# Optimization experiments

Measured on AMD Instinct MI355X. Metric: run time of the kernel, lower is better.

The kernel has to match this reference:

```python
import jax, jax.numpy as jnp
import numpy as np

NEG = -100.0
# Transition index layout from DecoderPHMM cat order
M2M, M2I, M2D, I2M, I2I, D2M, D2D = 0, 1, 2, 3, 4, 5, 6
LOG_QUARTER = float(np.log(0.25))


def _d_chain(fM, a):
    """Delete-state recurrence along motif axis k for one sequence column.
    fD[0] = NEG; fD[k] = logaddexp(a[k-1,M2D] + fM[k-1], a[k-1,D2D] + fD[k-1]).
    fM: (B, K+1), a: (B, K+1, 7) -> (B, K+1)."""
    B, Kp1 = fM.shape
    K = Kp1 - 1

    def step(fD_prev, inp):
        am2d, ad2d, fMk = inp  # each (B,)
        fD = jnp.logaddexp(am2d + fMk, ad2d + fD_prev)
        return fD, fD

    init = jnp.full((B,), NEG, dtype=fM.dtype)
    inputs = (a[:, :K, M2D].T, a[:, :K, D2D].T, fM[:, :K].T)  # (K, B) each
    _, fDs = jax.lax.scan(step, init, inputs)
    return jnp.concatenate([init[:, None], fDs.T], axis=1)  # (B, K+1)


def _profile_hmm_loss(transition_probs, emission_probs, batch_input):
    """Profile-HMM forward algorithm in log space, vectorized over batch.
    transition_probs: (B, K+1, 7) log; emission_probs: (B, K, 4) log;
    batch_input: (B, L) int tokens in [0,4). Returns (B,) NLL."""
    a = transition_probs
    e_m = emission_probs
    B, Kp1, _ = a.shape
    K = Kp1 - 1
    b_idx = jnp.arange(B)
    k_idx = jnp.arange(K)

    # Column l = 0: f[M,0,0] = 0, rest -100; I stays -100; D chain over k.
    fM0 = jnp.full((B, Kp1), NEG, dtype=a.dtype).at[:, 0].set(0.0)
    fI0 = jnp.full((B, Kp1), NEG, dtype=a.dtype)
    fD0 = _d_chain(fM0, a)

    def col_step(carry, sym):
        fM, fI, fD = carry  # each (B, K+1), previous column l-1
        # emission e_m[b, k, sym[b]] -> (B, K)
        em = e_m[b_idx[:, None], k_idx[None, :], sym[:, None]]
        prev = jnp.stack([a[:, :K, M2M] + fM[:, :K],
                          a[:, :K, I2M] + fI[:, :K],
                          a[:, :K, D2M] + fD[:, :K]], axis=0)  # (3, B, K)
        fM_new = jnp.concatenate(
            [jnp.full((B, 1), NEG, dtype=a.dtype),
             em + jax.scipy.special.logsumexp(prev, axis=0)], axis=1)
        fI_new = LOG_QUARTER + jnp.logaddexp(a[:, :, M2I] + fM,
                                             a[:, :, I2I] + fI)
        fD_new = _d_chain(fM_new, a)  # uses current-column M values
        return (fM_new, fI_new, fD_new), None

    (fM, fI, fD), _ = jax.lax.scan(col_step, (fM0, fI0, fD0), batch_input.T)

    final = jnp.stack([fM[:, K] + a[:, K, M2M],
                       fI[:, K] + a[:, K, I2M],
                       fD[:, K] + a[:, K, D2M]], axis=0)  # (3, B)
    return -jax.scipy.special.logsumexp(final, axis=0)


def _kld_loss(mus, logvars):
    return -0.5 * jnp.sum(1.0 + logvars - mus ** 2 - jnp.exp(logvars), axis=1)


def setup_inputs() -> dict:
    key = jax.random.key(0)
    k1, k2, k3, k4, k5 = jax.random.split(key, 5)
    B, L, K, E = 512, 256, 128, 16
    batch_input = jax.random.randint(k1, (B, L), 0, 4)
    transition_probs = jax.random.normal(k2, (B, K + 1, 7), dtype=jnp.float32)
    emission_probs = jax.random.normal(k3, (B, K, 4), dtype=jnp.float32)
    mus = jax.random.normal(k4, (B, E), dtype=jnp.float32)
    logvars = jax.random.normal(k5, (B, E), dtype=jnp.float32)
    return {"batch_input": batch_input, "transition_probs": transition_probs,
            "emission_probs": emission_probs, "mus": mus, "logvars": logvars}


def reference(batch_input, transition_probs, emission_probs, mus, logvars):
    beta = 1.0
    recon = _profile_hmm_loss(transition_probs, emission_probs, batch_input).mean()
    kld = _kld_loss(mus, logvars).mean()
    return recon + beta * kld
```

## Files before the change

kernel.cpp:

```cpp
#include <hip/hip_runtime.h>


constexpr float LOG2E = 1.4426950408889634f;
constexpr float LN2   = 0.6931471805599453f;

__device__ __forceinline__ float exp2_hw(float x){ return __builtin_amdgcn_exp2f(x); }
__device__ __forceinline__ float log2_hw(float x){ return __builtin_amdgcn_logf(x); }
__device__ __forceinline__ float ldx(float x,int e){ return __builtin_amdgcn_ldexpf(x,e); }
__device__ __forceinline__ int   fxe(float x){ return __builtin_amdgcn_frexp_expf(x); }
__device__ __forceinline__ int   dppi(int o,int s){ return __builtin_amdgcn_update_dpp(o,s,0x138,0xF,0xF,false); }
__device__ __forceinline__ float dppf(float o,float s){ return __int_as_float(dppi(__float_as_int(o),__float_as_int(s))); }

#define STEP(FRESH, ISS1, MASKED, SM1) do {                                    \
                    \
    const float qmM = dppf(0.0f, emM);              \
    const float qmI = dppf(0.0f, emI);                                         \
    const float qmD = dppf(0.0f, emD);                                         \
    const float qeM = dppf(0.0f, cMy);              \
    const float qeI = dppf(0.0f, cIy);                                         \
    const float qeD = dppf(0.0f, cDy);                                         \
    const int   qE  = dppi(E, E);          \
    const int qsym  = dppi((FRESH), symq);                                     \
                \
    const float v   = (ISS1) ? q1g : gg * u;                    \
    const float nI1 = fmaf(tmi1, cMx, tii1 * cIx);                             \
    const float nI2 = fmaf(tmi2, cMy, tii2 * cIy);                             \
    const float sq  = ldx(1.0f, qE - E);                                       \
    const float sp  = ldx(1.0f, pE - E);                                       \
    const float tPI = ldx(u, EI0 - E);               \
    const float tmI = ldx(v, EI0 - E);                                         \
                  \
    const float mM  = qmM * sq;                          \
    const float mD  = qmD * sq;                                                \
    const float eM_ = qeM * sq;                                                \
    const float eD_ = qeD * sq;                                                \
    const float PM  = pM * sp;             \
    const float PD  = pD * sp;                                                 \
    const float mI  = lane0 ? tmI : qmI * sq;                                  \
    const float PI  = lane0 ? tPI : pI * sp;                                   \
                                               \
    const bool ba = (qsym & 1) != 0, bb = (qsym & 2) != 0;                     \
    const bool bc = (qsym & 4) != 0, bd = (qsym & 8) != 0;                     \
    const float e1c = bb ? (ba ? el1.w : el1.z) : (ba ? el1.y : el1.x);        \
    const float e2c = bb ? (ba ? el2.w : el2.z) : (ba ? el2.y : el2.x);        \
    const float e1d = bd ? (bc ? el1.w : el1.z) : (bc ? el1.y : el1.x);        \
    const float e2d = bd ? (bc ? el2.w : el2.z) : (bc ? el2.y : el2.x);        \
                                                          \
    const float nM1 = e1c * fmaf(tdm0, PD,  fmaf(tim0, PI,  tmm0 * PM));       \
    const float nM2 = e2c * fmaf(tdm1, cDx, fmaf(tim1, cIx, tmm1 * cMx));      \
    const float nD1 = fmaf(tmd0, mM, tdd0 * mD);                               \
    const float nD2 = fmaf(tmd1, nM1, tdd1 * nD1);                             \
                                                        \
    const float nM1b = e1d * fmaf(tdm0, mD,  fmaf(tim0, mI,  tmm0 * mM));      \
    const float nI1b = fmaf(tmi1, nM1, tii1 * nI1);                            \
    const float nI2b = fmaf(tmi2, nM2, tii2 * nI2);                            \
    const float nD1b = fmaf(tmd0, eM_, tdd0 * eD_);                            \
    const float nM2b = e2d * fmaf(tdm1, nD1, fmaf(tim1, nI1, tmm1 * nM1));     \
    const float nD2b = fmaf(tmd1, nM1b, tdd1 * nD1b);                          \
                                                         \
    emM = nM2; emI = nI2; emD = nD2;               \
    if (MASKED) {                                                              \
        const bool act = ((unsigned)((SM1) - i)) < 128u;                       \
        cMx = act ? nM1b : cMx;  cMy = act ? nM2b : cMy;                       \
        cIx = act ? nI1b : cIx;  cIy = act ? nI2b : cIy;                       \
        cDx = act ? nD1b : cDx;  cDy = act ? nD2b : cDy;                       \
    } else {                                                                   \
        cMx = nM1b; cMy = nM2b; cIx = nI1b; cIy = nI2b; cDx = nD1b; cDy = nD2b;\
    }                                                                          \
    pM = qeM; pI = qeI; pD = qeD; pE = qE;                                     \
    symq = qsym;                                                               \
    u = gg * v;                                                   \
} while (0)

#define RESCALE do {                                                           \
    const float anc = fmaxf(fmaxf(fmaxf(cMx, cMy), fmaxf(cIx, cIy)),           \
                            fmaxf(cDx, cDy));                                  \
    const int e = fxe(anc);                                                    \
    E += e;                                                                    \
    const float sE = ldx(1.0f, -e);                                            \
    cMx *= sE; cMy *= sE; cIx *= sE; cIy *= sE; cDx *= sE; cDy *= sE;          \
    emM *= sE; emI *= sE; emD *= sE;                                           \
    const int eI = fxe(u); EI0 += eI; u = ldx(u, -eI);                         \
} while (0)

__global__ __launch_bounds__(64, 1) void phmm_fwd(const int* __restrict__ tokens,
                                                  const float* __restrict__ trans,
                                                  const float* __restrict__ emis,
                                                  float* __restrict__ nll_out)
{
    const int b = blockIdx.x;
    const int i = threadIdx.x;
    const bool lane0 = (i == 0);

    const float* ab = trans + (size_t)b * 903;
    const int r0 = (2*i)*7, r1 = (2*i+1)*7, r2 = (2*i+2)*7;

    const float tmm0 = exp2_hw(ab[r0+0]*LOG2E);
    const float tim0 = exp2_hw(ab[r0+3]*LOG2E);
    const float tdm0 = exp2_hw(ab[r0+5]*LOG2E);
    const float tmd0 = exp2_hw(ab[r0+2]*LOG2E);
    const float tdd0 = exp2_hw(ab[r0+6]*LOG2E);
    const float tmm1 = exp2_hw(ab[r1+0]*LOG2E);
    const float tim1 = exp2_hw(ab[r1+3]*LOG2E);
    const float tdm1 = exp2_hw(ab[r1+5]*LOG2E);
    const float tmd1 = exp2_hw(ab[r1+2]*LOG2E);
    const float tdd1 = exp2_hw(ab[r1+6]*LOG2E);
    const float tmi1 = 0.25f*exp2_hw(ab[r1+1]*LOG2E);
    const float tii1 = 0.25f*exp2_hw(ab[r1+4]*LOG2E);
    const float tmi2 = 0.25f*exp2_hw(ab[r2+1]*LOG2E);
    const float tii2 = 0.25f*exp2_hw(ab[r2+4]*LOG2E);
    const float q1g  = 0.25f*exp2_hw(ab[1]*LOG2E);
    const float gg   = 0.25f*exp2_hw(ab[4]*LOG2E);
    const float tKmm = exp2_hw(ab[128*7+0]*LOG2E);
    const float tKim = exp2_hw(ab[128*7+3]*LOG2E);
    const float tKdm = exp2_hw(ab[128*7+5]*LOG2E);

    const float4* eb = (const float4*)(emis + (size_t)b*512);
    float4 el1 = eb[2*i], el2 = eb[2*i+1];
    el1.x=exp2_hw(el1.x*LOG2E); el1.y=exp2_hw(el1.y*LOG2E);
    el1.z=exp2_hw(el1.z*LOG2E); el1.w=exp2_hw(el1.w*LOG2E);
    el2.x=exp2_hw(el2.x*LOG2E); el2.y=exp2_hw(el2.y*LOG2E);
    el2.z=exp2_hw(el2.z*LOG2E); el2.w=exp2_hw(el2.w*LOG2E);

    const int4 ts = ((const int4*)(tokens + (size_t)b*256))[i];

    const float ldd0 = ab[r0+6]*LOG2E;
    const float ldd1 = ab[r1+6]*LOG2E;
    const float lmd0b = ab[2]*LOG2E;
    float incl = (lane0 ? 0.0f : ldd0) + ldd1;
    #pragma unroll
    for (int d = 1; d < 64; d <<= 1) {
        float t = __shfl_up(incl, d);
        if (i >= d) incl += t;
    }
    float exPre = __shfl_up(incl, 1);
    if (lane0) exPre = 0.0f;
    const float g1 = lmd0b + exPre + (lane0 ? 0.0f : ldd0);
    const float g2 = g1 + ldd1;

    int E = (int)floorf(fmaxf(g1, g2));
    float cMx = 0.0f, cMy = 0.0f, cIx = 0.0f, cIy = 0.0f;
    float cDx = exp2_hw(g1 - (float)E), cDy = exp2_hw(g2 - (float)E);
    float emM = 0.0f, emI = 0.0f, emD = 0.0f;
    float pM = lane0 ? 1.0f : 0.0f;
    float pI = 0.0f, pD = 0.0f; int pE = 0;
    float u = 0.0f; int EI0 = 0;
    int symq = 0;

    #pragma unroll 1
    for (int g = 0; g < 16; ++g) {
        const int a0 = __builtin_amdgcn_readlane(ts.x, 2*g);
        const int a1 = __builtin_amdgcn_readlane(ts.y, 2*g);
        const int a2 = __builtin_amdgcn_readlane(ts.z, 2*g);
        const int a3 = __builtin_amdgcn_readlane(ts.w, 2*g);
        const int b0 = __builtin_amdgcn_readlane(ts.x, 2*g+1);
        const int b1 = __builtin_amdgcn_readlane(ts.y, 2*g+1);
        const int b2 = __builtin_amdgcn_readlane(ts.z, 2*g+1);
        const int b3 = __builtin_amdgcn_readlane(ts.w, 2*g+1);
        STEP(a0 | (a1 << 2), g == 0, 1, 4*g);
        STEP(a2 | (a3 << 2), false,  1, 4*g + 1);
        STEP(b0 | (b1 << 2), false,  1, 4*g + 2);
        STEP(b2 | (b3 << 2), false,  1, 4*g + 3);
        RESCALE;
    }
    #pragma unroll 1
    for (int g = 16; g < 32; ++g) {
        const int a0 = __builtin_amdgcn_readlane(ts.x, 2*g);
        const int a1 = __builtin_amdgcn_readlane(ts.y, 2*g);
        const int a2 = __builtin_amdgcn_readlane(ts.z, 2*g);
        const int a3 = __builtin_amdgcn_readlane(ts.w, 2*g);
        const int b0 = __builtin_amdgcn_readlane(ts.x, 2*g+1);
        const int b1 = __builtin_amdgcn_readlane(ts.y, 2*g+1);
        const int b2 = __builtin_amdgcn_readlane(ts.z, 2*g+1);
        const int b3 = __builtin_amdgcn_readlane(ts.w, 2*g+1);
        STEP(a0 | (a1 << 2), false, 0, 4*g);
        STEP(a2 | (a3 << 2), false, 0, 4*g + 1);
        STEP(b0 | (b1 << 2), false, 0, 4*g + 2);
        STEP(b2 | (b3 << 2), false, 0, 4*g + 3);
        RESCALE;
    }
    #pragma unroll 1
    for (int g = 32; g < 48; ++g) {
        STEP(0, false, 1, 4*g);
        STEP(0, false, 1, 4*g + 1);
        STEP(0, false, 1, 4*g + 2);
        STEP(0, false, 1, 4*g + 3);
        RESCALE;
    }

    const float fin = fmaf(tKdm, cDy, fmaf(tKim, cIy, tKmm*cMy));
    if (i == 63) nll_out[b] = -(log2_hw(fin) + (float)E)*LN2;
}

__global__ __launch_bounds__(256) void phmm_finish(const float* __restrict__ nll,
                                                   const float* __restrict__ mus,
                                                   const float* __restrict__ logvars,
                                                   float* __restrict__ out)
{
    const int tid = threadIdx.x;
    float acc = 0.0f;
    for (int idx = tid; idx < 512; idx += 256) acc += nll[idx];
    for (int idx = tid; idx < 8192; idx += 256) {
        const float mu = mus[idx], lv = logvars[idx];
        acc -= 0.5f * (1.0f + lv - mu * mu - exp2_hw(lv * LOG2E));
    }
    #pragma unroll
    for (int off = 32; off >= 1; off >>= 1) acc += __shfl_down(acc, off);
    __shared__ float red[4];
    if ((tid & 63) == 0) red[tid >> 6] = acc;
    __syncthreads();
    if (tid == 0) out[0] = (red[0] + red[1] + red[2] + red[3]) * (1.0f / 512.0f);
}

extern "C" void kernel_launch(void* const* d_in, const int* in_sizes, int n_in,
                              void* d_out, int out_size, void* d_ws, size_t ws_size,
                              hipStream_t stream)
{
    const int*   tokens  = (const int*)d_in[0];
    const float* trans   = (const float*)d_in[1];
    const float* emis    = (const float*)d_in[2];
    const float* mus     = (const float*)d_in[3];
    const float* logvars = (const float*)d_in[4];
    float* nll = (float*)d_ws;

    phmm_fwd<<<dim3(512), dim3(64), 0, stream>>>(tokens, trans, emis, nll);
    phmm_finish<<<dim3(1), dim3(256), 0, stream>>>(nll, mus, logvars, (float*)d_out);
}
```

Before: 42.68 us.

## Process two sequences per wavefront using packed float2 math

Each 64-lane block now runs the forward recurrence for two batch elements at once, holding state in two-wide float vectors so the compiler can emit packed FP32 instructions (v_pk_fma_f32). The grid is halved from 512 to 256 blocks. The aim is to spread the serial DPP/latency chain over twice the work per instruction and rely on packed math throughput. In exchange, register pressure roughly doubles, and with only 256 single-wave blocks, fewer of the 256 CUs' SIMDs are busy, so the per-block serial latency may grow.

```diff
diff --git a/kernel.cpp b/kernel.cpp
--- a/kernel.cpp
+++ b/kernel.cpp
@@ -1,5 +1,7 @@
 #include <hip/hip_runtime.h>
 
+
+typedef float v2f __attribute__((ext_vector_type(2)));
 
 constexpr float LOG2E = 1.4426950408889634f;
 constexpr float LN2   = 0.6931471805599453f;
@@ -10,53 +12,59 @@
 __device__ __forceinline__ int   fxe(float x){ return __builtin_amdgcn_frexp_expf(x); }
 __device__ __forceinline__ int   dppi(int o,int s){ return __builtin_amdgcn_update_dpp(o,s,0x138,0xF,0xF,false); }
 __device__ __forceinline__ float dppf(float o,float s){ return __int_as_float(dppi(__float_as_int(o),__float_as_int(s))); }
+__device__ __forceinline__ v2f   dppv(v2f s){ v2f r; r.x = dppf(0.0f, s.x); r.y = dppf(0.0f, s.y); return r; }
+__device__ __forceinline__ float esel(const float4 e, int s){
+    const float lo = (s & 1) ? e.y : e.x;
+    const float hi = (s & 1) ? e.w : e.z;
+    return (s & 2) ? hi : lo;
+}
 
 #define STEP(FRESH, ISS1, MASKED, SM1) do {                                    \
-                    \
-    const float qmM = dppf(0.0f, emM);              \
-    const float qmI = dppf(0.0f, emI);                                         \
-    const float qmD = dppf(0.0f, emD);                                         \
-    const float qeM = dppf(0.0f, cMy);              \
-    const float qeI = dppf(0.0f, cIy);                                         \
-    const float qeD = dppf(0.0f, cDy);                                         \
-    const int   qE  = dppi(E, E);          \
-    const int qsym  = dppi((FRESH), symq);                                     \
-                \
-    const float v   = (ISS1) ? q1g : gg * u;                    \
-    const float nI1 = fmaf(tmi1, cMx, tii1 * cIx);                             \
-    const float nI2 = fmaf(tmi2, cMy, tii2 * cIy);                             \
-    const float sq  = ldx(1.0f, qE - E);                                       \
-    const float sp  = ldx(1.0f, pE - E);                                       \
-    const float tPI = ldx(u, EI0 - E);               \
-    const float tmI = ldx(v, EI0 - E);                                         \
-                  \
-    const float mM  = qmM * sq;                          \
-    const float mD  = qmD * sq;                                                \
-    const float eM_ = qeM * sq;                                                \
-    const float eD_ = qeD * sq;                                                \
-    const float PM  = pM * sp;             \
-    const float PD  = pD * sp;                                                 \
-    const float mI  = lane0 ? tmI : qmI * sq;                                  \
-    const float PI  = lane0 ? tPI : pI * sp;                                   \
-                                               \
-    const bool ba = (qsym & 1) != 0, bb = (qsym & 2) != 0;                     \
-    const bool bc = (qsym & 4) != 0, bd = (qsym & 8) != 0;                     \
-    const float e1c = bb ? (ba ? el1.w : el1.z) : (ba ? el1.y : el1.x);        \
-    const float e2c = bb ? (ba ? el2.w : el2.z) : (ba ? el2.y : el2.x);        \
-    const float e1d = bd ? (bc ? el1.w : el1.z) : (bc ? el1.y : el1.x);        \
-    const float e2d = bd ? (bc ? el2.w : el2.z) : (bc ? el2.y : el2.x);        \
+                                 \
+    const v2f qmM = dppv(emM);                      \
+    const v2f qmI = dppv(emI);                                                 \
+    const v2f qmD = dppv(emD);                                                 \
+    const v2f qeM = dppv(cMy);                      \
+    const v2f qeI = dppv(cIy);                                                 \
+    const v2f qeD = dppv(cDy);                                                 \
+    const int qE0 = dppi(E0, E0);              \
+    const int qE1 = dppi(E1, E1);                                              \
+    const int qsym = dppi((FRESH), symq);                                      \
+                         \
+    const v2f v   = (ISS1) ? q1g : gg * u;                      \
+    const v2f nI1 = tmi1 * cMx + tii1 * cIx;                                   \
+    const v2f nI2 = tmi2 * cMy + tii2 * cIy;                                   \
+    v2f sqv; sqv.x = ldx(1.0f, qE0 - E0); sqv.y = ldx(1.0f, qE1 - E1);         \
+    v2f spv; spv.x = ldx(1.0f, pE0 - E0); spv.y = ldx(1.0f, pE1 - E1);         \
+    v2f tPI; tPI.x = ldx(u.x, EI00 - E0); tPI.y = ldx(u.y, EI01 - E1);         \
+    v2f tmIv; tmIv.x = ldx(v.x, EI00 - E0); tmIv.y = ldx(v.y, EI01 - E1);      \
+                                              \
+    const v2f mM  = qmM * sqv;                           \
+    const v2f mD  = qmD * sqv;                                                 \
+    const v2f eM_ = qeM * sqv;                                                 \
+    const v2f eD_ = qeD * sqv;                                                 \
+    const v2f PM  = pM * spv;              \
+    const v2f PD  = pD * spv;                                                  \
+    v2f mI = qmI * sqv, PI = pI * spv;                                         \
+    if (lane0) { mI = tmIv; PI = tPI; }                                        \
+                      \
+    const int sA = qsym & 15, sB = (qsym >> 8) & 15;                           \
+    v2f e1c; e1c.x = esel(el1A, sA & 3);        e1c.y = esel(el1B, sB & 3);    \
+    v2f e2c; e2c.x = esel(el2A, sA & 3);        e2c.y = esel(el2B, sB & 3);    \
+    v2f e1d; e1d.x = esel(el1A, (sA >> 2) & 3); e1d.y = esel(el1B, (sB >> 2) & 3); \
+    v2f e2d; e2d.x = esel(el2A, (sA >> 2) & 3); e2d.y = esel(el2B, (sB >> 2) & 3); \
                                                           \
-    const float nM1 = e1c * fmaf(tdm0, PD,  fmaf(tim0, PI,  tmm0 * PM));       \
-    const float nM2 = e2c * fmaf(tdm1, cDx, fmaf(tim1, cIx, tmm1 * cMx));      \
-    const float nD1 = fmaf(tmd0, mM, tdd0 * mD);                               \
-    const float nD2 = fmaf(tmd1, nM1, tdd1 * nD1);                             \
+    const v2f nM1 = e1c * (tdm0 * PD  + (tim0 * PI  + tmm0 * PM));             \
+    const v2f nM2 = e2c * (tdm1 * cDx + (tim1 * cIx + tmm1 * cMx));            \
+    const v2f nD1 = tmd0 * mM + tdd0 * mD;                                     \
+    const v2f nD2 = tmd1 * nM1 + tdd1 * nD1;                                   \
                                                         \
-    const float nM1b = e1d * fmaf(tdm0, mD,  fmaf(tim0, mI,  tmm0 * mM));      \
-    const float nI1b = fmaf(tmi1, nM1, tii1 * nI1);                            \
-    const float nI2b = fmaf(tmi2, nM2, tii2 * nI2);                            \
-    const float nD1b = fmaf(tmd0, eM_, tdd0 * eD_);                            \
-    const float nM2b = e2d * fmaf(tdm1, nD1, fmaf(tim1, nI1, tmm1 * nM1));     \
-    const float nD2b = fmaf(tmd1, nM1b, tdd1 * nD1b);                          \
+    const v2f nM1b = e1d * (tdm0 * mD  + (tim0 * mI  + tmm0 * mM));            \
+    const v2f nI1b = tmi1 * nM1 + tii1 * nI1;                                  \
+    const v2f nI2b = tmi2 * nM2 + tii2 * nI2;                                  \
+    const v2f nD1b = tmd0 * eM_ + tdd0 * eD_;                                  \
+    const v2f nM2b = e2d * (tdm1 * nD1 + (tim1 * nI1 + tmm1 * nM1));           \
+    const v2f nD2b = tmd1 * nM1b + tdd1 * nD1b;                                \
                                                          \
     emM = nM2; emI = nI2; emD = nD2;               \
     if (MASKED) {                                                              \
@@ -67,20 +75,24 @@
     } else {                                                                   \
         cMx = nM1b; cMy = nM2b; cIx = nI1b; cIy = nI2b; cDx = nD1b; cDy = nD2b;\
     }                                                                          \
-    pM = qeM; pI = qeI; pD = qeD; pE = qE;                                     \
+    pM = qeM; pI = qeI; pD = qeD; pE0 = qE0; pE1 = qE1;                        \
     symq = qsym;                                                               \
     u = gg * v;                                                   \
 } while (0)
 
 #define RESCALE do {                                                           \
-    const float anc = fmaxf(fmaxf(fmaxf(cMx, cMy), fmaxf(cIx, cIy)),           \
-                            fmaxf(cDx, cDy));                                  \
-    const int e = fxe(anc);                                                    \
-    E += e;                                                                    \
-    const float sE = ldx(1.0f, -e);                                            \
+    const float ancA = fmaxf(fmaxf(fmaxf(cMx.x, cMy.x), fmaxf(cIx.x, cIy.x)),  \
+                             fmaxf(cDx.x, cDy.x));                             \
+    const float ancB = fmaxf(fmaxf(fmaxf(cMx.y, cMy.y), fmaxf(cIx.y, cIy.y)),  \
+                             fmaxf(cDx.y, cDy.y));                             \
+    const int eA = fxe(ancA), eB = fxe(ancB);                                  \
+    E0 += eA; E1 += eB;                                                        \
+    v2f sE; sE.x = ldx(1.0f, -eA); sE.y = ldx(1.0f, -eB);                      \
     cMx *= sE; cMy *= sE; cIx *= sE; cIy *= sE; cDx *= sE; cDy *= sE;          \
     emM *= sE; emI *= sE; emD *= sE;                                           \
-    const int eI = fxe(u); EI0 += eI; u = ldx(u, -eI);                         \
+    const int eIA = fxe(u.x); EI00 += eIA;                                     \
+    const int eIB = fxe(u.y); EI01 += eIB;                                     \
+    u.x = ldx(u.x, -eIA); u.y = ldx(u.y, -eIB);                                \
 } while (0)
 
 __global__ __launch_bounds__(64, 1) void phmm_fwd(const int* __restrict__ tokens,
@@ -92,91 +104,114 @@
     const int i = threadIdx.x;
     const bool lane0 = (i == 0);
 
-    const float* ab = trans + (size_t)b * 903;
+    const float* abA = trans + (size_t)(2*b) * 903;
+    const float* abB = trans + (size_t)(2*b+1) * 903;
     const int r0 = (2*i)*7, r1 = (2*i+1)*7, r2 = (2*i+2)*7;
 
-    const float tmm0 = exp2_hw(ab[r0+0]*LOG2E);
-    const float tim0 = exp2_hw(ab[r0+3]*LOG2E);
-    const float tdm0 = exp2_hw(ab[r0+5]*LOG2E);
-    const float tmd0 = exp2_hw(ab[r0+2]*LOG2E);
-    const float tdd0 = exp2_hw(ab[r0+6]*LOG2E);
-    const float tmm1 = exp2_hw(ab[r1+0]*LOG2E);
-    const float tim1 = exp2_hw(ab[r1+3]*LOG2E);
-    const float tdm1 = exp2_hw(ab[r1+5]*LOG2E);
-    const float tmd1 = exp2_hw(ab[r1+2]*LOG2E);
-    const float tdd1 = exp2_hw(ab[r1+6]*LOG2E);
-    const float tmi1 = 0.25f*exp2_hw(ab[r1+1]*LOG2E);
-    const float tii1 = 0.25f*exp2_hw(ab[r1+4]*LOG2E);
-    const float tmi2 = 0.25f*exp2_hw(ab[r2+1]*LOG2E);
-    const float tii2 = 0.25f*exp2_hw(ab[r2+4]*LOG2E);
-    const float q1g  = 0.25f*exp2_hw(ab[1]*LOG2E);
-    const float gg   = 0.25f*exp2_hw(ab[4]*LOG2E);
-    const float tKmm = exp2_hw(ab[128*7+0]*LOG2E);
-    const float tKim = exp2_hw(ab[128*7+3]*LOG2E);
-    const float tKdm = exp2_hw(ab[128*7+5]*LOG2E);
-
-    const float4* eb = (const float4*)(emis + (size_t)b*512);
-    float4 el1 = eb[2*i], el2 = eb[2*i+1];
-    el1.x=exp2_hw(el1.x*LOG2E); el1.y=exp2_hw(el1.y*LOG2E);
-    el1.z=exp2_hw(el1.z*LOG2E); el1.w=exp2_hw(el1.w*LOG2E);
-    el2.x=exp2_hw(el2.x*LOG2E); el2.y=exp2_hw(el2.y*LOG2E);
-    el2.z=exp2_hw(el2.z*LOG2E); el2.w=exp2_hw(el2.w*LOG2E);
-
-    const int4 ts = ((const int4*)(tokens + (size_t)b*256))[i];
-
-    const float ldd0 = ab[r0+6]*LOG2E;
-    const float ldd1 = ab[r1+6]*LOG2E;
-    const float lmd0b = ab[2]*LOG2E;
-    float incl = (lane0 ? 0.0f : ldd0) + ldd1;
+#define LD2(expr_r) (v2f){ exp2_hw(abA[expr_r]*LOG2E), exp2_hw(abB[expr_r]*LOG2E) }
+    const v2f tmm0 = LD2(r0+0), tim0 = LD2(r0+3), tdm0 = LD2(r0+5);
+    const v2f tmd0 = LD2(r0+2), tdd0 = LD2(r0+6);
+    const v2f tmm1 = LD2(r1+0), tim1 = LD2(r1+3), tdm1 = LD2(r1+5);
+    const v2f tmd1 = LD2(r1+2), tdd1 = LD2(r1+6);
+    const v2f tmi1 = 0.25f*LD2(r1+1), tii1 = 0.25f*LD2(r1+4);
+    const v2f tmi2 = 0.25f*LD2(r2+1), tii2 = 0.25f*LD2(r2+4);
+    const v2f q1g  = 0.25f*LD2(1), gg = 0.25f*LD2(4);
+    const v2f tKmm = LD2(128*7+0), tKim = LD2(128*7+3), tKdm = LD2(128*7+5);
+#undef LD2
+
+    const float4* ebA = (const float4*)(emis + (size_t)(2*b)*512);
+    const float4* ebB = (const float4*)(emis + (size_t)(2*b+1)*512);
+    float4 el1A = ebA[2*i], el2A = ebA[2*i+1];
+    float4 el1B = ebB[2*i], el2B = ebB[2*i+1];
+    el1A.x=exp2_hw(el1A.x*LOG2E); el1A.y=exp2_hw(el1A.y*LOG2E);
+    el1A.z=exp2_hw(el1A.z*LOG2E); el1A.w=exp2_hw(el1A.w*LOG2E);
+    el2A.x=exp2_hw(el2A.x*LOG2E); el2A.y=exp2_hw(el2A.y*LOG2E);
+    el2A.z=exp2_hw(el2A.z*LOG2E); el2A.w=exp2_hw(el2A.w*LOG2E);
+    el1B.x=exp2_hw(el1B.x*LOG2E); el1B.y=exp2_hw(el1B.y*LOG2E);
+    el1B.z=exp2_hw(el1B.z*LOG2E); el1B.w=exp2_hw(el1B.w*LOG2E);
+    el2B.x=exp2_hw(el2B.x*LOG2E); el2B.y=exp2_hw(el2B.y*LOG2E);
+    el2B.z=exp2_hw(el2B.z*LOG2E); el2B.w=exp2_hw(el2B.w*LOG2E);
+
+    const int4 tsA = ((const int4*)(tokens + (size_t)(2*b)*256))[i];
+    const int4 tsB = ((const int4*)(tokens + (size_t)(2*b+1)*256))[i];
+
+    const float ldd0A = abA[r0+6]*LOG2E, ldd1A = abA[r1+6]*LOG2E;
+    const float ldd0B = abB[r0+6]*LOG2E, ldd1B = abB[r1+6]*LOG2E;
+    float inclA = (lane0 ? 0.0f : ldd0A) + ldd1A;
+    float inclB = (lane0 ? 0.0f : ldd0B) + ldd1B;
     #pragma unroll
     for (int d = 1; d < 64; d <<= 1) {
-        float t = __shfl_up(incl, d);
-        if (i >= d) incl += t;
-    }
-    float exPre = __shfl_up(incl, 1);
-    if (lane0) exPre = 0.0f;
-    const float g1 = lmd0b + exPre + (lane0 ? 0.0f : ldd0);
-    const float g2 = g1 + ldd1;
-
-    int E = (int)floorf(fmaxf(g1, g2));
-    float cMx = 0.0f, cMy = 0.0f, cIx = 0.0f, cIy = 0.0f;
-    float cDx = exp2_hw(g1 - (float)E), cDy = exp2_hw(g2 - (float)E);
-    float emM = 0.0f, emI = 0.0f, emD = 0.0f;
-    float pM = lane0 ? 1.0f : 0.0f;
-    float pI = 0.0f, pD = 0.0f; int pE = 0;
-    float u = 0.0f; int EI0 = 0;
+        const float tA = __shfl_up(inclA, d);
+        const float tB = __shfl_up(inclB, d);
+        if (i >= d) { inclA += tA; inclB += tB; }
+    }
+    float exPreA = __shfl_up(inclA, 1);
+    float exPreB = __shfl_up(inclB, 1);
+    if (lane0) { exPreA = 0.0f; exPreB = 0.0f; }
+    const float g1A = abA[2]*LOG2E + exPreA + (lane0 ? 0.0f : ldd0A);
+    const float g2A = g1A + ldd1A;
+    const float g1B = abB[2]*LOG2E + exPreB + (lane0 ? 0.0f : ldd0B);
+    const float g2B = g1B + ldd1B;
+
+    int E0 = (int)floorf(fmaxf(g1A, g2A));
+    int E1 = (int)floorf(fmaxf(g1B, g2B));
+    v2f cMx = {0,0}, cMy = {0,0}, cIx = {0,0}, cIy = {0,0};
+    v2f cDx; cDx.x = exp2_hw(g1A - (float)E0); cDx.y = exp2_hw(g1B - (float)E1);
+    v2f cDy; cDy.x = exp2_hw(g2A - (float)E0); cDy.y = exp2_hw(g2B - (float)E1);
+    v2f emM = {0,0}, emI = {0,0}, emD = {0,0};
+    v2f pM = lane0 ? (v2f){1.0f,1.0f} : (v2f){0,0};
+    v2f pI = {0,0}, pD = {0,0};
+    int pE0 = 0, pE1 = 0;
+    v2f u = {0,0};
+    int EI00 = 0, EI01 = 0;
     int symq = 0;
 
     #pragma unroll 1
     for (int g = 0; g < 16; ++g) {
-        const int a0 = __builtin_amdgcn_readlane(ts.x, 2*g);
-        const int a1 = __builtin_amdgcn_readlane(ts.y, 2*g);
-        const int a2 = __builtin_amdgcn_readlane(ts.z, 2*g);
-        const int a3 = __builtin_amdgcn_readlane(ts.w, 2*g);
-        const int b0 = __builtin_amdgcn_readlane(ts.x, 2*g+1);
-        const int b1 = __builtin_amdgcn_readlane(ts.y, 2*g+1);
-        const int b2 = __builtin_amdgcn_readlane(ts.z, 2*g+1);
-        const int b3 = __builtin_amdgcn_readlane(ts.w, 2*g+1);
-        STEP(a0 | (a1 << 2), g == 0, 1, 4*g);
-        STEP(a2 | (a3 << 2), false,  1, 4*g + 1);
-        STEP(b0 | (b1 << 2), false,  1, 4*g + 2);
-        STEP(b2 | (b3 << 2), false,  1, 4*g + 3);
+        const int a0A = __builtin_amdgcn_readlane(tsA.x, 2*g);
+        const int a1A = __builtin_amdgcn_readlane(tsA.y, 2*g);
+        const int a2A = __builtin_amdgcn_readlane(tsA.z, 2*g);
+        const int a3A = __builtin_amdgcn_readlane(tsA.w, 2*g);
+        const int b0A = __builtin_amdgcn_readlane(tsA.x, 2*g+1);
+        const int b1A = __builtin_amdgcn_readlane(tsA.y, 2*g+1);
+        const int b2A = __builtin_amdgcn_readlane(tsA.z, 2*g+1);
+        const int b3A = __builtin_amdgcn_readlane(tsA.w, 2*g+1);
+        const int a0B = __builtin_amdgcn_readlane(tsB.x, 2*g);
+        const int a1B = __builtin_amdgcn_readlane(tsB.y, 2*g);
+        const int a2B = __builtin_amdgcn_readlane(tsB.z, 2*g);
+        const int a3B = __builtin_amdgcn_readlane(tsB.w, 2*g);
+        const int b0B = __builtin_amdgcn_readlane(tsB.x, 2*g+1);
+        const int b1B = __builtin_amdgcn_readlane(tsB.y, 2*g+1);
+        const int b2B = __builtin_amdgcn_readlane(tsB.z, 2*g+1);
+        const int b3B = __builtin_amdgcn_readlane(tsB.w, 2*g+1);
+        STEP((a0A|(a1A<<2)) | ((a0B|(a1B<<2))<<8), g == 0, 1, 4*g);
+        STEP((a2A|(a3A<<2)) | ((a2B|(a3B<<2))<<8), false,  1, 4*g + 1);
+        STEP((b0A|(b1A<<2)) | ((b0B|(b1B<<2))<<8), false,  1, 4*g + 2);
+        STEP((b2A|(b3A<<2)) | ((b2B|(b3B<<2))<<8), false,  1, 4*g + 3);
         RESCALE;
     }
     #pragma unroll 1
     for (int g = 16; g < 32; ++g) {
-        const int a0 = __builtin_amdgcn_readlane(ts.x, 2*g);
-        const int a1 = __builtin_amdgcn_readlane(ts.y, 2*g);
-        const int a2 = __builtin_amdgcn_readlane(ts.z, 2*g);
-        const int a3 = __builtin_amdgcn_readlane(ts.w, 2*g);
-        const int b0 = __builtin_amdgcn_readlane(ts.x, 2*g+1);
-        const int b1 = __builtin_amdgcn_readlane(ts.y, 2*g+1);
-        const int b2 = __builtin_amdgcn_readlane(ts.z, 2*g+1);
-        const int b3 = __builtin_amdgcn_readlane(ts.w, 2*g+1);
-        STEP(a0 | (a1 << 2), false, 0, 4*g);
-        STEP(a2 | (a3 << 2), false, 0, 4*g + 1);
-        STEP(b0 | (b1 << 2), false, 0, 4*g + 2);
-        STEP(b2 | (b3 << 2), false, 0, 4*g + 3);
+        const int a0A = __builtin_amdgcn_readlane(tsA.x, 2*g);
+        const int a1A = __builtin_amdgcn_readlane(tsA.y, 2*g);
+        const int a2A = __builtin_amdgcn_readlane(tsA.z, 2*g);
+        const int a3A = __builtin_amdgcn_readlane(tsA.w, 2*g);
+        const int b0A = __builtin_amdgcn_readlane(tsA.x, 2*g+1);
+        const int b1A = __builtin_amdgcn_readlane(tsA.y, 2*g+1);
+        const int b2A = __builtin_amdgcn_readlane(tsA.z, 2*g+1);
+        const int b3A = __builtin_amdgcn_readlane(tsA.w, 2*g+1);
+        const int a0B = __builtin_amdgcn_readlane(tsB.x, 2*g);
+        const int a1B = __builtin_amdgcn_readlane(tsB.y, 2*g);
+        const int a2B = __builtin_amdgcn_readlane(tsB.z, 2*g);
+        const int a3B = __builtin_amdgcn_readlane(tsB.w, 2*g);
+        const int b0B = __builtin_amdgcn_readlane(tsB.x, 2*g+1);
+        const int b1B = __builtin_amdgcn_readlane(tsB.y, 2*g+1);
+        const int b2B = __builtin_amdgcn_readlane(tsB.z, 2*g+1);
+        const int b3B = __builtin_amdgcn_readlane(tsB.w, 2*g+1);
+        STEP((a0A|(a1A<<2)) | ((a0B|(a1B<<2))<<8), false, 0, 4*g);
+        STEP((a2A|(a3A<<2)) | ((a2B|(a3B<<2))<<8), false, 0, 4*g + 1);
+        STEP((b0A|(b1A<<2)) | ((b0B|(b1B<<2))<<8), false, 0, 4*g + 2);
+        STEP((b2A|(b3A<<2)) | ((b2B|(b3B<<2))<<8), false, 0, 4*g + 3);
         RESCALE;
     }
     #pragma unroll 1
@@ -188,8 +223,11 @@
         RESCALE;
     }
 
-    const float fin = fmaf(tKdm, cDy, fmaf(tKim, cIy, tKmm*cMy));
-    if (i == 63) nll_out[b] = -(log2_hw(fin) + (float)E)*LN2;
+    const v2f fin = tKdm * cDy + (tKim * cIy + tKmm * cMy);
+    if (i == 63) {
+        nll_out[2*b]   = -(log2_hw(fin.x) + (float)E0) * LN2;
+        nll_out[2*b+1] = -(log2_hw(fin.y) + (float)E1) * LN2;
+    }
 }
 
 __global__ __launch_bounds__(256) void phmm_finish(const float* __restrict__ nll,
@@ -223,6 +261,6 @@
     const float* logvars = (const float*)d_in[4];
     float* nll = (float*)d_ws;
 
-    phmm_fwd<<<dim3(512), dim3(64), 0, stream>>>(tokens, trans, emis, nll);
+    phmm_fwd<<<dim3(256), dim3(64), 0, stream>>>(tokens, trans, emis, nll);
     phmm_finish<<<dim3(1), dim3(256), 0, stream>>>(nll, mus, logvars, (float*)d_out);
 }
```

After: 64.26 us. 1.51x slower.

## Precompute neighbor-lane transition combos before DPP exchange in PHMM wavefront

Applied to the files above, without the earlier changes.

Each lane now combines its boundary-state values with the next row's transition weights before the cross-lane shift. This cuts the per-step DPP transfers from eight to five (four floats plus the symbol), and the receiving lane no longer evaluates those transitions itself. The scale-exponent exchange moves out of the step into once per group of four steps, and the final readout reuses the precomputed combination. The cost is a few extra FMAs on the sending lane. The change also relies on the exponent staying fixed within a group, which affects precision at lane boundaries.

```diff
diff --git a/kernel.cpp b/kernel.cpp
--- a/kernel.cpp
+++ b/kernel.cpp
@@ -12,33 +12,24 @@
 __device__ __forceinline__ float dppf(float o,float s){ return __int_as_float(dppi(__float_as_int(o),__float_as_int(s))); }
 
 #define STEP(FRESH, ISS1, MASKED, SM1) do {                                    \
-                    \
-    const float qmM = dppf(0.0f, emM);              \
-    const float qmI = dppf(0.0f, emI);                                         \
-    const float qmD = dppf(0.0f, emD);                                         \
-    const float qeM = dppf(0.0f, cMy);              \
-    const float qeI = dppf(0.0f, cIy);                                         \
-    const float qeD = dppf(0.0f, cDy);                                         \
-    const int   qE  = dppi(E, E);          \
-    const int qsym  = dppi((FRESH), symq);                                     \
-                \
+    const float qdMm = dppf(0.0f, xdMm);                                       \
+    const float qdMe = dppf(0.0f, xdMe);                                       \
+    const float qdDm = dppf(0.0f, xdDm);                                       \
+    const float qdDe = dppf(0.0f, xdDe);                                       \
+    const int   qsym = dppi((FRESH), symq);                                    \
     const float v   = (ISS1) ? q1g : gg * u;                    \
     const float nI1 = fmaf(tmi1, cMx, tii1 * cIx);                             \
     const float nI2 = fmaf(tmi2, cMy, tii2 * cIy);                             \
-    const float sq  = ldx(1.0f, qE - E);                                       \
-    const float sp  = ldx(1.0f, pE - E);                                       \
-    const float tPI = ldx(u, EI0 - E);               \
-    const float tmI = ldx(v, EI0 - E);                                         \
-                  \
-    const float mM  = qmM * sq;                          \
-    const float mD  = qmD * sq;                                                \
-    const float eM_ = qeM * sq;                                                \
-    const float eD_ = qeD * sq;                                                \
-    const float PM  = pM * sp;             \
-    const float PD  = pD * sp;                                                 \
-    const float mI  = lane0 ? tmI : qmI * sq;                                  \
-    const float PI  = lane0 ? tPI : pI * sp;                                   \
-                                               \
+    float dM_c1 = qdMm * sq;                                                   \
+    const float dD_c  = qdDm * sq;            \
+    const float dD_c1 = qdDe * sq;                                             \
+    const float dM_sv = qdMe * sq;                                             \
+    float dP = pdM;                                                            \
+          \
+    const float z0 = fmaf(tim0, ldx(u, EI0 - E),                               \
+                          (ISS1) ? ldx(tmm0, -E) : 0.0f);                      \
+    const float z1 = tim0 * ldx(v, EI0 - E);                                   \
+    if (lane0) { dP = z0; dM_c1 = z1; }                                        \
     const bool ba = (qsym & 1) != 0, bb = (qsym & 2) != 0;                     \
     const bool bc = (qsym & 4) != 0, bd = (qsym & 8) != 0;                     \
     const float e1c = bb ? (ba ? el1.w : el1.z) : (ba ? el1.y : el1.x);        \
@@ -46,28 +37,35 @@
     const float e1d = bd ? (bc ? el1.w : el1.z) : (bc ? el1.y : el1.x);        \
     const float e2d = bd ? (bc ? el2.w : el2.z) : (bc ? el2.y : el2.x);        \
                                                           \
-    const float nM1 = e1c * fmaf(tdm0, PD,  fmaf(tim0, PI,  tmm0 * PM));       \
+    const float nM1 = e1c * dP;                                                \
     const float nM2 = e2c * fmaf(tdm1, cDx, fmaf(tim1, cIx, tmm1 * cMx));      \
-    const float nD1 = fmaf(tmd0, mM, tdd0 * mD);                               \
+    const float nD1 = dD_c;                                                    \
     const float nD2 = fmaf(tmd1, nM1, tdd1 * nD1);                             \
                                                         \
-    const float nM1b = e1d * fmaf(tdm0, mD,  fmaf(tim0, mI,  tmm0 * mM));      \
+    const float nM1b = e1d * dM_c1;                                            \
     const float nI1b = fmaf(tmi1, nM1, tii1 * nI1);                            \
     const float nI2b = fmaf(tmi2, nM2, tii2 * nI2);                            \
-    const float nD1b = fmaf(tmd0, eM_, tdd0 * eD_);                            \
+    const float nD1b = dD_c1;                                                  \
     const float nM2b = e2d * fmaf(tdm1, nD1, fmaf(tim1, nI1, tmm1 * nM1));     \
     const float nD2b = fmaf(tmd1, nM1b, tdd1 * nD1b);                          \
+               \
+    const float ndMm = fmaf(t2mm, nM2,  fmaf(t2im, nI2,  t2dm * nD2));         \
+    const float ndMe = fmaf(t2mm, nM2b, fmaf(t2im, nI2b, t2dm * nD2b));        \
+    const float ndDm = fmaf(t2md, nM2,  t2dd * nD2);                           \
+    const float ndDe = fmaf(t2md, nM2b, t2dd * nD2b);                          \
                                                          \
-    emM = nM2; emI = nI2; emD = nD2;               \
+    xdMm = ndMm; xdDm = ndDm; xdDe = ndDe;       \
     if (MASKED) {                                                              \
         const bool act = ((unsigned)((SM1) - i)) < 128u;                       \
         cMx = act ? nM1b : cMx;  cMy = act ? nM2b : cMy;                       \
         cIx = act ? nI1b : cIx;  cIy = act ? nI2b : cIy;                       \
         cDx = act ? nD1b : cDx;  cDy = act ? nD2b : cDy;                       \
+        xdMe = act ? ndMe : xdMe;        \
     } else {                                                                   \
         cMx = nM1b; cMy = nM2b; cIx = nI1b; cIy = nI2b; cDx = nD1b; cDy = nD2b;\
+        xdMe = ndMe;                                                           \
     }                                                                          \
-    pM = qeM; pI = qeI; pD = qeD; pE = qE;                                     \
+    pdM = dM_sv;                                                               \
     symq = qsym;                                                               \
     u = gg * v;                                                   \
 } while (0)
@@ -79,7 +77,7 @@
     E += e;                                                                    \
     const float sE = ldx(1.0f, -e);                                            \
     cMx *= sE; cMy *= sE; cIx *= sE; cIy *= sE; cDx *= sE; cDy *= sE;          \
-    emM *= sE; emI *= sE; emD *= sE;                                           \
+    xdMm *= sE; xdMe *= sE; xdDm *= sE; xdDe *= sE; pdM *= sE;                 \
     const int eI = fxe(u); EI0 += eI; u = ldx(u, -eI);                         \
 } while (0)
 
@@ -97,9 +95,6 @@
 
     const float tmm0 = exp2_hw(ab[r0+0]*LOG2E);
     const float tim0 = exp2_hw(ab[r0+3]*LOG2E);
-    const float tdm0 = exp2_hw(ab[r0+5]*LOG2E);
-    const float tmd0 = exp2_hw(ab[r0+2]*LOG2E);
-    const float tdd0 = exp2_hw(ab[r0+6]*LOG2E);
     const float tmm1 = exp2_hw(ab[r1+0]*LOG2E);
     const float tim1 = exp2_hw(ab[r1+3]*LOG2E);
     const float tdm1 = exp2_hw(ab[r1+5]*LOG2E);
@@ -109,11 +104,13 @@
     const float tii1 = 0.25f*exp2_hw(ab[r1+4]*LOG2E);
     const float tmi2 = 0.25f*exp2_hw(ab[r2+1]*LOG2E);
     const float tii2 = 0.25f*exp2_hw(ab[r2+4]*LOG2E);
+    const float t2mm = exp2_hw(ab[r2+0]*LOG2E);
+    const float t2im = exp2_hw(ab[r2+3]*LOG2E);
+    const float t2dm = exp2_hw(ab[r2+5]*LOG2E);
+    const float t2md = exp2_hw(ab[r2+2]*LOG2E);
+    const float t2dd = exp2_hw(ab[r2+6]*LOG2E);
     const float q1g  = 0.25f*exp2_hw(ab[1]*LOG2E);
     const float gg   = 0.25f*exp2_hw(ab[4]*LOG2E);
-    const float tKmm = exp2_hw(ab[128*7+0]*LOG2E);
-    const float tKim = exp2_hw(ab[128*7+3]*LOG2E);
-    const float tKdm = exp2_hw(ab[128*7+5]*LOG2E);
 
     const float4* eb = (const float4*)(emis + (size_t)b*512);
     float4 el1 = eb[2*i], el2 = eb[2*i+1];
@@ -141,14 +138,16 @@
     int E = (int)floorf(fmaxf(g1, g2));
     float cMx = 0.0f, cMy = 0.0f, cIx = 0.0f, cIy = 0.0f;
     float cDx = exp2_hw(g1 - (float)E), cDy = exp2_hw(g2 - (float)E);
-    float emM = 0.0f, emI = 0.0f, emD = 0.0f;
-    float pM = lane0 ? 1.0f : 0.0f;
-    float pI = 0.0f, pD = 0.0f; int pE = 0;
+    float xdMm = 0.0f, xdDm = 0.0f, xdDe = 0.0f;
+    float xdMe = t2dm * cDy;
+    float pdM = 0.0f;
     float u = 0.0f; int EI0 = 0;
     int symq = 0;
 
     #pragma unroll 1
     for (int g = 0; g < 16; ++g) {
+        const int qE = dppi(E, E);
+        const float sq = ldx(1.0f, qE - E);
         const int a0 = __builtin_amdgcn_readlane(ts.x, 2*g);
         const int a1 = __builtin_amdgcn_readlane(ts.y, 2*g);
         const int a2 = __builtin_amdgcn_readlane(ts.z, 2*g);
@@ -165,6 +164,8 @@
     }
     #pragma unroll 1
     for (int g = 16; g < 32; ++g) {
+        const int qE = dppi(E, E);
+        const float sq = ldx(1.0f, qE - E);
         const int a0 = __builtin_amdgcn_readlane(ts.x, 2*g);
         const int a1 = __builtin_amdgcn_readlane(ts.y, 2*g);
         const int a2 = __builtin_amdgcn_readlane(ts.z, 2*g);
@@ -181,6 +182,8 @@
     }
     #pragma unroll 1
     for (int g = 32; g < 48; ++g) {
+        const int qE = dppi(E, E);
+        const float sq = ldx(1.0f, qE - E);
         STEP(0, false, 1, 4*g);
         STEP(0, false, 1, 4*g + 1);
         STEP(0, false, 1, 4*g + 2);
@@ -188,8 +191,7 @@
         RESCALE;
     }
 
-    const float fin = fmaf(tKdm, cDy, fmaf(tKim, cIy, tKmm*cMy));
-    if (i == 63) nll_out[b] = -(log2_hw(fin) + (float)E)*LN2;
+    if (i == 63) nll_out[b] = -(log2_hw(xdMe) + (float)E)*LN2;
 }
 
 __global__ __launch_bounds__(256) void phmm_finish(const float* __restrict__ nll,
```

Measured after the change: 40.79 us. 1.05x faster.
